# Optimization experiments

Hardware: AMD Instinct MI355X
Metric: run time of the kernel (lower is better)

The kernel has to match this reference:

```python
import jax, jax.numpy as jnp
import numpy as np

D_MODEL = 1024
N_HEADS = 16
B, T = 2, 2048


def setup_inputs() -> dict:
    key = jax.random.key(0)
    kx, kqkv, ko = jax.random.split(key, 3)
    x = jax.random.normal(kx, (B, T, D_MODEL), dtype=jnp.float32)
    # flax Linear default init (lecun_normal ~ scaled); plain scaled normal is fine for a baseline
    Wqkv = jax.random.normal(kqkv, (D_MODEL, 3 * D_MODEL), dtype=jnp.float32) / np.sqrt(D_MODEL)
    Wo = jax.random.normal(ko, (D_MODEL, D_MODEL), dtype=jnp.float32) / np.sqrt(D_MODEL)
    return {"x": x, "Wqkv": Wqkv, "Wo": Wo}


def reference(x, Wqkv, Wo):
    Bx, Tx, C = x.shape
    H = N_HEADS
    Hd = C // H
    scale = C ** (-0.5)  # NOTE: module scales by d_model**-0.5, not head_dim**-0.5
    qkv = x @ Wqkv  # [B, T, 3C]
    q, k, v = jnp.split(qkv, 3, axis=-1)
    q = q.reshape(Bx, Tx, H, Hd).transpose(0, 2, 1, 3)  # [B,H,T,Hd]
    k = k.reshape(Bx, Tx, H, Hd).transpose(0, 2, 1, 3)
    v = v.reshape(Bx, Tx, H, Hd).transpose(0, 2, 1, 3)
    attn = jnp.einsum('bhid,bhjd->bhij', q, k) * scale  # [B,H,T,T]
    mask = jnp.tril(jnp.ones((Tx, Tx), dtype=jnp.bool_))
    attn = jnp.where(mask[None, None], attn, jnp.finfo(attn.dtype).min)
    attn = jax.nn.softmax(attn.astype(jnp.float32), axis=-1).astype(attn.dtype)
    out = jnp.einsum('bhij,bhjd->bhid', attn, v)  # [B,H,T,Hd]
    out = out.transpose(0, 2, 1, 3).reshape(Bx, Tx, C)
    return out @ Wo
```

## Files before the change

### kernel.cpp

```cpp
#include <hip/hip_runtime.h>
#include <cstdint>
#include <math.h>

#define D_MODEL 1024
#define N_HEADS 16
#define HEAD_DIM 64
#define BB 2
#define TT 2048
#define QSCALE 0.04508422002778011f
#define MSTATIC 12.0f

typedef float f32x4 __attribute__((ext_vector_type(4)));
typedef __bf16 bf16x8 __attribute__((ext_vector_type(8)));

__device__ inline ushort f2bf(float f) {
    union { float f; uint32_t u; } c; c.f = f;
    uint32_t u = c.u;
    uint32_t r = (u + 0x7FFFu + ((u >> 16) & 1u)) >> 16;
    return (ushort)r;
}
__device__ inline ushort f2bf_hw(float f) {
    __bf16 h = (__bf16)f;
    return __builtin_bit_cast(ushort, h);
}

__device__ inline void load_lds16(const ushort* g, ushort* lds_uniform_base) {
    __builtin_amdgcn_global_load_lds(
        (const __attribute__((address_space(1))) uint32_t*)g,
        (__attribute__((address_space(3))) uint32_t*)lds_uniform_base, 16, 0, 0);
}

__global__ __launch_bounds__(256) void conv_x(
    const float4* __restrict__ in, ushort4* __restrict__ out, int n4)
{
    int i = blockIdx.x * 256 + threadIdx.x;
    if (i < n4) {
        float4 v = in[i];
        ushort4 u;
        u.x = f2bf(v.x); u.y = f2bf(v.y); u.z = f2bf(v.z); u.w = f2bf(v.w);
        out[i] = u;
    }
}

__global__ __launch_bounds__(256) void transpose_f32_bf16(
    const float* __restrict__ in, ushort* __restrict__ out, int R, int C)
{
    __shared__ ushort tile[32][33];
    int tx = threadIdx.x;
    int ty = threadIdx.y;
    int c0 = blockIdx.x * 32;
    int r0 = blockIdx.y * 32;
#pragma unroll
    for (int i = 0; i < 32; i += 8)
        tile[ty + i][tx] = f2bf(in[(size_t)(r0 + ty + i) * C + (c0 + tx)]);
    __syncthreads();
#pragma unroll
    for (int i = 0; i < 32; i += 8)
        out[(size_t)(c0 + ty + i) * R + (r0 + tx)] = tile[tx][ty + i];
}

__device__ inline void gemm128_mainloop(
    const ushort* __restrict__ A, const ushort* __restrict__ BT,
    int rowBase, int colBase, ushort* Al, ushort* Bl,
    f32x4 acc[4][4], int wave, int lane)
{
    const int K = D_MODEL;
    int lr = lane & 15, quad = lane >> 4;
    int lrow = lane >> 2;
    int kq = lane & 3;
    int mq = (wave >> 1) * 64, nq = (wave & 1) * 64;

    const ushort* gA0 = A + (size_t)(rowBase + wave * 32 + lrow) * K + kq * 8;
    const ushort* gA1 = gA0 + (size_t)16 * K;
    const ushort* gB0 = BT + (size_t)(colBase + wave * 32 + lrow) * K + kq * 8;
    const ushort* gB1 = gB0 + (size_t)16 * K;
    ushort* lA0 = Al + (wave * 32) * 32;
    ushort* lA1 = Al + (wave * 32 + 16) * 32;
    ushort* lB0 = Bl + (wave * 32) * 32;
    ushort* lB1 = Bl + (wave * 32 + 16) * 32;

    for (int kt = 0; kt < K / 32; ++kt) {
        __syncthreads();
        int ko = kt * 32;
        load_lds16(gA0 + ko, lA0);
        load_lds16(gA1 + ko, lA1);
        load_lds16(gB0 + ko, lB0);
        load_lds16(gB1 + ko, lB1);
        __syncthreads();
        bf16x8 af[4], bf[4];
#pragma unroll
        for (int mi = 0; mi < 4; ++mi)
            af[mi] = *(const bf16x8*)(Al + (mq + mi * 16 + lr) * 32 + quad * 8);
#pragma unroll
        for (int ni = 0; ni < 4; ++ni)
            bf[ni] = *(const bf16x8*)(Bl + (nq + ni * 16 + lr) * 32 + quad * 8);
#pragma unroll
        for (int mi = 0; mi < 4; ++mi)
#pragma unroll
            for (int ni = 0; ni < 4; ++ni)
                acc[mi][ni] = __builtin_amdgcn_mfma_f32_16x16x32_bf16(
                    af[mi], bf[ni], acc[mi][ni], 0, 0, 0);
    }
}

__global__ __launch_bounds__(256) void gemm_qkv(
    const ushort* __restrict__ A, const ushort* __restrict__ BT,
    ushort* __restrict__ Qo, ushort* __restrict__ Ko, ushort* __restrict__ VTo)
{
    __shared__ ushort Al[128 * 32];
    __shared__ ushort Bl[128 * 32];
    int tid = threadIdx.x;
    int wave = tid >> 6, lane = tid & 63;
    int lr = lane & 15, quad = lane >> 4;
    int rowBase = blockIdx.y * 128;
    int colBase = blockIdx.x * 128;
    f32x4 acc[4][4] = {};
    gemm128_mainloop(A, BT, rowBase, colBase, Al, Bl, acc, wave, lane);

    int mq = (wave >> 1) * 64, nq = (wave & 1) * 64;
#pragma unroll
    for (int ni = 0; ni < 4; ++ni) {
        int n = colBase + nq + ni * 16 + lr;
        int s = n >> 10;
        int cc = n & 1023;
        int h = cc >> 6, d = cc & 63;
        float scale = (s == 0) ? QSCALE : 1.0f;
#pragma unroll
        for (int mi = 0; mi < 4; ++mi) {
#pragma unroll
            for (int i = 0; i < 4; ++i) {
                int m = rowBase + mq + mi * 16 + quad * 4 + i;
                int b = m >> 11, t = m & 2047;
                int bh = b * N_HEADS + h;
                if (s == 2) {
                    VTo[((size_t)bh * HEAD_DIM + d) * TT + t] = f2bf(acc[mi][ni][i]);
                } else {
                    ushort* dst = (s == 0) ? Qo : Ko;
                    dst[((size_t)bh * TT + t) * HEAD_DIM + d] = f2bf(acc[mi][ni][i] * scale);
                }
            }
        }
    }
}

__global__ __launch_bounds__(256) void gemm_plain(
    const ushort* __restrict__ A, const ushort* __restrict__ BT,
    float* __restrict__ O, int N)
{
    __shared__ ushort Al[128 * 32];
    __shared__ ushort Bl[128 * 32];
    int tid = threadIdx.x;
    int wave = tid >> 6, lane = tid & 63;
    int lr = lane & 15, quad = lane >> 4;
    int rowBase = blockIdx.y * 128;
    int colBase = blockIdx.x * 128;
    f32x4 acc[4][4] = {};
    gemm128_mainloop(A, BT, rowBase, colBase, Al, Bl, acc, wave, lane);

    int mq = (wave >> 1) * 64, nq = (wave & 1) * 64;
#pragma unroll
    for (int mi = 0; mi < 4; ++mi)
#pragma unroll
        for (int ni = 0; ni < 4; ++ni) {
            int n = colBase + nq + ni * 16 + lr;
#pragma unroll
            for (int i = 0; i < 4; ++i) {
                int m = rowBase + mq + mi * 16 + quad * 4 + i;
                O[(size_t)m * N + n] = acc[mi][ni][i];
            }
        }
}

__global__ __launch_bounds__(512) void attn_flash(
    const ushort* __restrict__ Q,
    const ushort* __restrict__ K,
    const ushort* __restrict__ VT,
    ushort* __restrict__ AO)
{
    int bid = blockIdx.x;
    int bh  = bid & 31;
    int idx = bid >> 5;
    int qi  = (idx < 8) ? idx : (23 - idx);
    int tid = threadIdx.x;
    int wave = tid >> 6;
    int pair = wave & 3;
    int half = wave >> 2;
    int lane = tid & 63;
    int quad = lane >> 4, lr = lane & 15;
    int qw = qi * 128 + pair * 32;

    const ushort* Qb = Q  + (size_t)bh * TT * HEAD_DIM;
    const ushort* Kb = K  + (size_t)bh * TT * HEAD_DIM;
    const ushort* Vb = VT + (size_t)bh * HEAD_DIM * TT;

    __shared__ ushort pbuf[8][32][40];
    __shared__ float comb[4][10][64][4];
    ushort (*P)[40] = pbuf[wave];

    bf16x8 qa[2][2];
#pragma unroll
    for (int r = 0; r < 2; ++r)
#pragma unroll
        for (int s = 0; s < 2; ++s)
            qa[r][s] = *(const bf16x8*)(Qb + (size_t)(qw + r * 16 + lr) * HEAD_DIM
                                           + s * 32 + quad * 8);

    f32x4 o[2][4] = {};
    f32x4 l[2] = {};

    bf16x8 ones;
#pragma unroll
    for (int j = 0; j < 8; ++j) ones[j] = (__bf16)1.0f;

    int ktiles = (qw >> 5) + 1;
    for (int kt = half; kt < ktiles; kt += 2) {
        int k0 = kt << 5;
        bf16x8 kb[2][2];
#pragma unroll
        for (int c = 0; c < 2; ++c)
#pragma unroll
            for (int s = 0; s < 2; ++s)
                kb[c][s] = *(const bf16x8*)(Kb + (size_t)(k0 + c * 16 + lr) * HEAD_DIM
                                               + s * 32 + quad * 8);
        f32x4 sc[2][2];
#pragma unroll
        for (int r = 0; r < 2; ++r)
#pragma unroll
            for (int c = 0; c < 2; ++c)
#pragma unroll
                for (int i = 0; i < 4; ++i) sc[r][c][i] = -MSTATIC;
#pragma unroll
        for (int r = 0; r < 2; ++r)
#pragma unroll
            for (int c = 0; c < 2; ++c) {
                sc[r][c] = __builtin_amdgcn_mfma_f32_16x16x32_bf16(qa[r][0], kb[c][0], sc[r][c], 0, 0, 0);
                sc[r][c] = __builtin_amdgcn_mfma_f32_16x16x32_bf16(qa[r][1], kb[c][1], sc[r][c], 0, 0, 0);
            }
        if (kt == ktiles - 1) {
#pragma unroll
            for (int r = 0; r < 2; ++r)
#pragma unroll
                for (int c = 0; c < 2; ++c)
#pragma unroll
                    for (int i = 0; i < 4; ++i)
                        if (c * 16 + lr > r * 16 + quad * 4 + i) sc[r][c][i] = -3e38f;
        }
        bf16x8 vb[4];
#pragma unroll
        for (int d = 0; d < 4; ++d)
            vb[d] = *(const bf16x8*)(Vb + (size_t)(d * 16 + lr) * TT + k0 + quad * 8);

#pragma unroll
        for (int r = 0; r < 2; ++r)
#pragma unroll
            for (int c = 0; c < 2; ++c)
#pragma unroll
                for (int i = 0; i < 4; ++i)
                    P[r * 16 + quad * 4 + i][c * 16 + lr] =
                        f2bf_hw(__builtin_amdgcn_exp2f(sc[r][c][i]));

#pragma unroll
        for (int r = 0; r < 2; ++r) {
            bf16x8 pa = *(const bf16x8*)&P[r * 16 + lr][quad * 8];
            l[r] = __builtin_amdgcn_mfma_f32_16x16x32_bf16(pa, ones, l[r], 0, 0, 0);
#pragma unroll
            for (int d = 0; d < 4; ++d)
                o[r][d] = __builtin_amdgcn_mfma_f32_16x16x32_bf16(pa, vb[d], o[r][d], 0, 0, 0);
        }
    }

    if (half == 1) {
#pragma unroll
        for (int r = 0; r < 2; ++r)
#pragma unroll
            for (int d = 0; d < 4; ++d)
                *(f32x4*)&comb[pair][r * 4 + d][lane][0] = o[r][d];
#pragma unroll
        for (int r = 0; r < 2; ++r)
            *(f32x4*)&comb[pair][8 + r][lane][0] = l[r];
    }
    __syncthreads();
    if (half == 0) {
#pragma unroll
        for (int r = 0; r < 2; ++r)
#pragma unroll
            for (int d = 0; d < 4; ++d)
                o[r][d] += *(const f32x4*)&comb[pair][r * 4 + d][lane][0];
#pragma unroll
        for (int r = 0; r < 2; ++r)
            l[r] += *(const f32x4*)&comb[pair][8 + r][lane][0];

        int b = bh >> 4, h = bh & 15;
#pragma unroll
        for (int r = 0; r < 2; ++r) {
            f32x4 rl;
#pragma unroll
            for (int i = 0; i < 4; ++i) rl[i] = 1.0f / l[r][i];
#pragma unroll
            for (int d = 0; d < 4; ++d)
#pragma unroll
                for (int i = 0; i < 4; ++i) {
                    int row = qw + r * 16 + quad * 4 + i;
                    AO[((size_t)(b * TT + row)) * D_MODEL + h * HEAD_DIM + d * 16 + lr] =
                        f2bf(o[r][d][i] * rl[i]);
                }
        }
    }
}

extern "C" void kernel_launch(void* const* d_in, const int* in_sizes, int n_in,
                              void* d_out, int out_size, void* d_ws, size_t ws_size,
                              hipStream_t stream)
{
    (void)in_sizes; (void)n_in; (void)out_size; (void)ws_size;
    const float* x    = (const float*)d_in[0];
    const float* Wqkv = (const float*)d_in[1];
    const float* Wo   = (const float*)d_in[2];
    float* out = (float*)d_out;

    char* ws = (char*)d_ws;
    size_t off = 0;
    ushort* WqkvT = (ushort*)(ws + off); off += (size_t)3 * D_MODEL * D_MODEL * 2;
    ushort* WoT   = (ushort*)(ws + off); off += (size_t)D_MODEL * D_MODEL * 2;
    ushort* xb    = (ushort*)(ws + off); off += (size_t)BB * TT * D_MODEL * 2;
    ushort* Qd    = (ushort*)(ws + off); off += (size_t)BB * D_MODEL * TT * 2;
    ushort* Kd    = (ushort*)(ws + off); off += (size_t)BB * D_MODEL * TT * 2;
    ushort* VTd   = (ushort*)(ws + off); off += (size_t)BB * D_MODEL * TT * 2;
    ushort* AO    = (ushort*)(ws + off); off += (size_t)BB * TT * D_MODEL * 2;

    int n4 = BB * TT * D_MODEL / 4;
    conv_x<<<dim3(n4 / 256), 256, 0, stream>>>(
        (const float4*)x, (ushort4*)xb, n4);

    transpose_f32_bf16<<<dim3(3 * D_MODEL / 32, D_MODEL / 32), dim3(32, 8), 0, stream>>>(
        Wqkv, WqkvT, D_MODEL, 3 * D_MODEL);
    transpose_f32_bf16<<<dim3(D_MODEL / 32, D_MODEL / 32), dim3(32, 8), 0, stream>>>(
        Wo, WoT, D_MODEL, D_MODEL);

    gemm_qkv<<<dim3(3 * D_MODEL / 128, BB * TT / 128), 256, 0, stream>>>(
        xb, WqkvT, Qd, Kd, VTd);

    attn_flash<<<dim3(512), 512, 0, stream>>>(Qd, Kd, VTd, AO);

    gemm_plain<<<dim3(D_MODEL / 128, BB * TT / 128), 256, 0, stream>>>(
        AO, WoT, out, D_MODEL);
}
```

Baseline: 235.9 us.

## Write V row-major then transpose separately; prefetch K/V in attention; narrow output GEMM tiles

The QKV GEMM now writes V in the same row-major layout as Q and K, replacing the strided scattered VT stores, and a new tiled LDS transpose kernel produces VT afterwards. The attention loop software-prefetches the next K and V fragments into registers one iteration ahead to hide global load latency. The output projection GEMM is switched to 128x64 tiles so more blocks run in parallel. In exchange there is an extra kernel launch, an extra V buffer in workspace, and higher register pressure in the attention kernel.

```diff
diff --git a/kernel.cpp b/kernel.cpp
--- a/kernel.cpp
+++ b/kernel.cpp
@@ -57,6 +57,25 @@
 #pragma unroll
     for (int i = 0; i < 32; i += 8)
         out[(size_t)(c0 + ty + i) * R + (r0 + tx)] = tile[tx][ty + i];
+}
+
+__global__ __launch_bounds__(256) void transpose_v_bf16(
+    const ushort* __restrict__ in, ushort* __restrict__ out)
+{
+    int z = blockIdx.z;
+    const ushort* ip = in + (size_t)z * TT * HEAD_DIM;
+    ushort* op = out + (size_t)z * TT * HEAD_DIM;
+    __shared__ ushort tile[32][33];
+    int tx = threadIdx.x, ty = threadIdx.y;
+    int d0 = blockIdx.x * 32;
+    int t0 = blockIdx.y * 32;
+#pragma unroll
+    for (int i = 0; i < 32; i += 8)
+        tile[ty + i][tx] = ip[(size_t)(t0 + ty + i) * HEAD_DIM + d0 + tx];
+    __syncthreads();
+#pragma unroll
+    for (int i = 0; i < 32; i += 8)
+        op[(size_t)(d0 + ty + i) * TT + t0 + tx] = tile[tx][ty + i];
 }
 
 __device__ inline void gemm128_mainloop(
@@ -105,7 +124,7 @@
 
 __global__ __launch_bounds__(256) void gemm_qkv(
     const ushort* __restrict__ A, const ushort* __restrict__ BT,
-    ushort* __restrict__ Qo, ushort* __restrict__ Ko, ushort* __restrict__ VTo)
+    ushort* __restrict__ Qo, ushort* __restrict__ Ko, ushort* __restrict__ Vo)
 {
     __shared__ ushort Al[128 * 32];
     __shared__ ushort Bl[128 * 32];
@@ -124,6 +143,7 @@
         int s = n >> 10;
         int cc = n & 1023;
         int h = cc >> 6, d = cc & 63;
+        ushort* dst = (s == 0) ? Qo : (s == 1 ? Ko : Vo);
         float scale = (s == 0) ? QSCALE : 1.0f;
 #pragma unroll
         for (int mi = 0; mi < 4; ++mi) {
@@ -132,12 +152,7 @@
                 int m = rowBase + mq + mi * 16 + quad * 4 + i;
                 int b = m >> 11, t = m & 2047;
                 int bh = b * N_HEADS + h;
-                if (s == 2) {
-                    VTo[((size_t)bh * HEAD_DIM + d) * TT + t] = f2bf(acc[mi][ni][i]);
-                } else {
-                    ushort* dst = (s == 0) ? Qo : Ko;
-                    dst[((size_t)bh * TT + t) * HEAD_DIM + d] = f2bf(acc[mi][ni][i] * scale);
-                }
+                dst[((size_t)bh * TT + t) * HEAD_DIM + d] = f2bf(acc[mi][ni][i] * scale);
             }
         }
     }
@@ -147,21 +162,56 @@
     const ushort* __restrict__ A, const ushort* __restrict__ BT,
     float* __restrict__ O, int N)
 {
+    const int K = D_MODEL;
     __shared__ ushort Al[128 * 32];
-    __shared__ ushort Bl[128 * 32];
+    __shared__ ushort Bl[64 * 32];
     int tid = threadIdx.x;
     int wave = tid >> 6, lane = tid & 63;
     int lr = lane & 15, quad = lane >> 4;
+    int lrow = lane >> 2, kq = lane & 3;
     int rowBase = blockIdx.y * 128;
-    int colBase = blockIdx.x * 128;
-    f32x4 acc[4][4] = {};
-    gemm128_mainloop(A, BT, rowBase, colBase, Al, Bl, acc, wave, lane);
-
-    int mq = (wave >> 1) * 64, nq = (wave & 1) * 64;
+    int colBase = blockIdx.x * 64;
+    int mq = (wave >> 1) * 64, nq = (wave & 1) * 32;
+
+    const ushort* gA0 = A + (size_t)(rowBase + wave * 32 + lrow) * K + kq * 8;
+    const ushort* gA1 = gA0 + (size_t)16 * K;
+    const ushort* gB0 = BT + (size_t)(colBase + wave * 32 + lrow) * K + kq * 8;
+    const ushort* gB1 = gB0 + (size_t)16 * K;
+    ushort* lA0 = Al + (wave * 32) * 32;
+    ushort* lA1 = Al + (wave * 32 + 16) * 32;
+    ushort* lB0 = Bl + (wave * 32) * 32;
+    ushort* lB1 = Bl + (wave * 32 + 16) * 32;
+
+    f32x4 acc[4][2] = {};
+    for (int kt = 0; kt < K / 32; ++kt) {
+        __syncthreads();
+        int ko = kt * 32;
+        load_lds16(gA0 + ko, lA0);
+        load_lds16(gA1 + ko, lA1);
+        if (wave < 2) {
+            load_lds16(gB0 + ko, lB0);
+            load_lds16(gB1 + ko, lB1);
+        }
+        __syncthreads();
+        bf16x8 af[4], bf[2];
+#pragma unroll
+        for (int mi = 0; mi < 4; ++mi)
+            af[mi] = *(const bf16x8*)(Al + (mq + mi * 16 + lr) * 32 + quad * 8);
+#pragma unroll
+        for (int ni = 0; ni < 2; ++ni)
+            bf[ni] = *(const bf16x8*)(Bl + (nq + ni * 16 + lr) * 32 + quad * 8);
+#pragma unroll
+        for (int mi = 0; mi < 4; ++mi)
+#pragma unroll
+            for (int ni = 0; ni < 2; ++ni)
+                acc[mi][ni] = __builtin_amdgcn_mfma_f32_16x16x32_bf16(
+                    af[mi], bf[ni], acc[mi][ni], 0, 0, 0);
+    }
+
 #pragma unroll
     for (int mi = 0; mi < 4; ++mi)
 #pragma unroll
-        for (int ni = 0; ni < 4; ++ni) {
+        for (int ni = 0; ni < 2; ++ni) {
             int n = colBase + nq + ni * 16 + lr;
 #pragma unroll
             for (int i = 0; i < 4; ++i) {
@@ -213,15 +263,43 @@
     for (int j = 0; j < 8; ++j) ones[j] = (__bf16)1.0f;
 
     int ktiles = (qw >> 5) + 1;
+    bf16x8 kbp[2][2], vbp[4];
+    if (half < ktiles) {
+        int k0 = half << 5;
+#pragma unroll
+        for (int c = 0; c < 2; ++c)
+#pragma unroll
+            for (int s = 0; s < 2; ++s)
+                kbp[c][s] = *(const bf16x8*)(Kb + (size_t)(k0 + c * 16 + lr) * HEAD_DIM
+                                                + s * 32 + quad * 8);
+#pragma unroll
+        for (int d = 0; d < 4; ++d)
+            vbp[d] = *(const bf16x8*)(Vb + (size_t)(d * 16 + lr) * TT + k0 + quad * 8);
+    }
+
     for (int kt = half; kt < ktiles; kt += 2) {
-        int k0 = kt << 5;
-        bf16x8 kb[2][2];
+        bf16x8 kb[2][2], vb[4];
 #pragma unroll
         for (int c = 0; c < 2; ++c)
 #pragma unroll
-            for (int s = 0; s < 2; ++s)
-                kb[c][s] = *(const bf16x8*)(Kb + (size_t)(k0 + c * 16 + lr) * HEAD_DIM
-                                               + s * 32 + quad * 8);
+            for (int s = 0; s < 2; ++s) kb[c][s] = kbp[c][s];
+#pragma unroll
+        for (int d = 0; d < 4; ++d) vb[d] = vbp[d];
+
+        int kn = kt + 2;
+        if (kn < ktiles) {
+            int k0n = kn << 5;
+#pragma unroll
+            for (int c = 0; c < 2; ++c)
+#pragma unroll
+                for (int s = 0; s < 2; ++s)
+                    kbp[c][s] = *(const bf16x8*)(Kb + (size_t)(k0n + c * 16 + lr) * HEAD_DIM
+                                                    + s * 32 + quad * 8);
+#pragma unroll
+            for (int d = 0; d < 4; ++d)
+                vbp[d] = *(const bf16x8*)(Vb + (size_t)(d * 16 + lr) * TT + k0n + quad * 8);
+        }
+
         f32x4 sc[2][2];
 #pragma unroll
         for (int r = 0; r < 2; ++r)
@@ -245,10 +323,6 @@
                     for (int i = 0; i < 4; ++i)
                         if (c * 16 + lr > r * 16 + quad * 4 + i) sc[r][c][i] = -3e38f;
         }
-        bf16x8 vb[4];
-#pragma unroll
-        for (int d = 0; d < 4; ++d)
-            vb[d] = *(const bf16x8*)(Vb + (size_t)(d * 16 + lr) * TT + k0 + quad * 8);
 
 #pragma unroll
         for (int r = 0; r < 2; ++r)
@@ -325,6 +399,7 @@
     ushort* xb    = (ushort*)(ws + off); off += (size_t)BB * TT * D_MODEL * 2;
     ushort* Qd    = (ushort*)(ws + off); off += (size_t)BB * D_MODEL * TT * 2;
     ushort* Kd    = (ushort*)(ws + off); off += (size_t)BB * D_MODEL * TT * 2;
+    ushort* Vd    = (ushort*)(ws + off); off += (size_t)BB * D_MODEL * TT * 2;
     ushort* VTd   = (ushort*)(ws + off); off += (size_t)BB * D_MODEL * TT * 2;
     ushort* AO    = (ushort*)(ws + off); off += (size_t)BB * TT * D_MODEL * 2;
 
@@ -338,10 +413,13 @@
         Wo, WoT, D_MODEL, D_MODEL);
 
     gemm_qkv<<<dim3(3 * D_MODEL / 128, BB * TT / 128), 256, 0, stream>>>(
-        xb, WqkvT, Qd, Kd, VTd);
+        xb, WqkvT, Qd, Kd, Vd);
+
+    transpose_v_bf16<<<dim3(HEAD_DIM / 32, TT / 32, BB * N_HEADS), dim3(32, 8), 0, stream>>>(
+        Vd, VTd);
 
     attn_flash<<<dim3(512), 512, 0, stream>>>(Qd, Kd, VTd, AO);
 
-    gemm_plain<<<dim3(D_MODEL / 128, BB * TT / 128), 256, 0, stream>>>(
+    gemm_plain<<<dim3(D_MODEL / 64, BB * TT / 128), 256, 0, stream>>>(
         AO, WoT, out, D_MODEL);
 }
```

Result: faster. 213.7 us (-9.4%).
